# Performance work log

Measured on AMD Instinct MI355X. Metric: run time of the kernel, lower is better.

The kernel has to match this reference:

```python
import jax, jax.numpy as jnp
import numpy as np
import math

H = 512
NH = 8
HD = H // NH


def _lin_params(key, out_dim, in_dim):
    k1, k2 = jax.random.split(key)
    bound = 1.0 / math.sqrt(in_dim)
    w = jax.random.uniform(k1, (out_dim, in_dim), minval=-bound, maxval=bound, dtype=jnp.float32)
    b = jax.random.uniform(k2, (out_dim,), minval=-bound, maxval=bound, dtype=jnp.float32)
    return w, b


def setup_inputs() -> dict:
    key = jax.random.key(0)
    ks = jax.random.split(key, 16)
    B, L = 8, 1024
    inp = {
        'hidden_states': jax.random.normal(ks[0], (B, L, H), dtype=jnp.float32),
        'text': jax.random.normal(ks[1], (B, L, H), dtype=jnp.float32),
    }
    names = ['q_img', 'k_img', 'v_img', 'q_txt', 'k_txt', 'v_txt', 'out_img', 'out_txt']
    for i, n in enumerate(names):
        w, b = _lin_params(ks[2 + i], H, H)
        inp['w_' + n] = w
        inp['b_' + n] = b
    wcat, bcat = _lin_params(ks[10], H, 2 * H)
    inp['w_cat'] = wcat
    inp['b_cat'] = bcat
    # nn.MultiheadAttention params: in_proj [3H, H], out_proj [H, H]
    inp['in_proj_w'] = jax.random.normal(ks[11], (3 * H, H), dtype=jnp.float32) * (1.0 / math.sqrt(H))
    inp['in_proj_b'] = jnp.zeros((3 * H,), dtype=jnp.float32)
    pw, pb = _lin_params(ks[12], H, H)
    inp['out_proj_w'] = pw
    inp['out_proj_b'] = pb
    return inp


def _lin(x, w, b):
    return x @ w.T + b


def _heads(x):
    B, L, _ = x.shape
    return x.reshape(B, L, NH, HD).transpose(0, 2, 1, 3)  # [B, NH, L, HD]


def _attn(q, k, v):
    # q,k,v: [B, NH, L, HD]; dropout is identity in eval mode
    scores = jnp.einsum('bhqd,bhkd->bhqk', q, k) / math.sqrt(HD)
    probs = jax.nn.softmax(scores, axis=-1)
    ctx = jnp.einsum('bhqk,bhkd->bhqd', probs, v)
    B, _, L, _ = ctx.shape
    return ctx.transpose(0, 2, 1, 3).reshape(B, L, H)


def reference(hidden_states, text,
              w_q_img, b_q_img, w_k_img, b_k_img, w_v_img, b_v_img,
              w_q_txt, b_q_txt, w_k_txt, b_k_txt, w_v_txt, b_v_txt,
              w_out_img, b_out_img, w_out_txt, b_out_txt,
              w_cat, b_cat, in_proj_w, in_proj_b, out_proj_w, out_proj_b):
    q_img = _heads(_lin(hidden_states, w_q_img, b_q_img))
    k_img = _heads(_lin(hidden_states, w_k_img, b_k_img))
    v_img = _heads(_lin(hidden_states, w_v_img, b_v_img))
    q_txt = _heads(_lin(text, w_q_txt, b_q_txt))
    k_txt = _heads(_lin(text, w_k_txt, b_k_txt))
    v_txt = _heads(_lin(text, w_v_txt, b_v_txt))

    ctx_img = _attn(q_img, k_img, v_img)
    ctx_txt = _attn(q_txt, k_txt, v_txt)
    ctx_it = _attn(q_img, k_txt, v_txt)
    ctx_ti = _attn(q_txt, k_img, v_img)

    out_img = _lin((ctx_img + ctx_it) * 0.5, w_out_img, b_out_img)
    out_txt = _lin((ctx_txt + ctx_ti) * 0.5, w_out_txt, b_out_txt)
    out = _lin(jnp.concatenate([out_img, out_txt], axis=2), w_cat, b_cat)

    # attention pooling (nn.MultiheadAttention self-attention, batch-major math)
    qkv = _lin(out, in_proj_w, in_proj_b)
    q, k, v = jnp.split(qkv, 3, axis=-1)
    ctx = _attn(_heads(q), _heads(k), _heads(v))
    return _lin(ctx, out_proj_w, out_proj_b)
```

## Files before the change

### kernel.cpp

```cpp
#include <hip/hip_runtime.h>

typedef unsigned short u16;
typedef __attribute__((ext_vector_type(4))) unsigned short u16x4;
typedef __attribute__((ext_vector_type(8))) unsigned short u16x8;
typedef __attribute__((ext_vector_type(4))) float f32x4;
typedef __attribute__((ext_vector_type(8))) __bf16 bf16x8;
typedef __attribute__((ext_vector_type(2))) unsigned int u32x2;
typedef __attribute__((ext_vector_type(4))) unsigned int u32x4;

#define WS_XH    0UL
#define WS_XT    8388608UL
#define WS_W     16777216UL
#define WS_BQI   24117248UL
#define WS_BQT   24123392UL
#define WS_QKVI  24129536UL
#define WS_QKVT  49295360UL
#define WS_VTI   74461184UL
#define WS_VTT   82849792UL
#define WS_CTXIA 91238400UL
#define WS_CTXTA 99627008UL
#define WS_OCAT  108015616UL
#define WS_OUT2  24129536UL
#define WS_QKVP  32518144UL
#define WS_VTP   57683968UL
#define WS_CTXP  66072576UL

#define SCALE_LOG2E_O8 0.18033688011112042f

__device__ __forceinline__ u16 f2bf(float f) {
  unsigned u = __float_as_uint(f);
  u += 0x7fffu + ((u >> 16) & 1u);
  return (u16)(u >> 16);
}
__device__ __forceinline__ float bf2f(u16 v) {
  return __uint_as_float(((unsigned)v) << 16);
}
__device__ __forceinline__ bf16x8 as_bf(u16x8 v) { return __builtin_bit_cast(bf16x8, v); }
__device__ __forceinline__ f32x4 mfma16(bf16x8 a, bf16x8 b, f32x4 c) {
  return __builtin_amdgcn_mfma_f32_16x16x32_bf16(a, b, c, 0, 0, 0);
}
__device__ __forceinline__ unsigned cvt_pk_bf16(float lo, float hi) {
  unsigned r;
  asm("v_cvt_pk_bf16_f32 %0, %1, %2" : "=v"(r) : "v"(lo), "v"(hi));
  return r;
}
__device__ __forceinline__ void gl_lds16(const u16* g, u16* l) {
  __builtin_amdgcn_global_load_lds(
      (const __attribute__((address_space(1))) void*)g,
      (__attribute__((address_space(3))) void*)l, 16, 0, 0);
}

__global__ __launch_bounds__(256) void cvt_f32_bf16(const float* __restrict__ s0,
                                                    const float* __restrict__ s1,
                                                    u16* __restrict__ d0,
                                                    u16* __restrict__ d1, int n) {
  const float* s = blockIdx.y ? s1 : s0;
  u16* d = blockIdx.y ? d1 : d0;
  int i = (blockIdx.x * 256 + threadIdx.x) * 4;
  if (i >= n) return;
  float4 v = *(const float4*)(s + i);
  u16x4 o;
  o[0] = f2bf(v.x); o[1] = f2bf(v.y); o[2] = f2bf(v.z); o[3] = f2bf(v.w);
  *(u16x4*)(d + i) = o;
}

__global__ __launch_bounds__(256) void prep_weights(
    const float* __restrict__ wqi, const float* __restrict__ wki, const float* __restrict__ wvi,
    const float* __restrict__ wqt, const float* __restrict__ wkt, const float* __restrict__ wvt,
    const float* __restrict__ woi, const float* __restrict__ wot,
    const float* __restrict__ wc,  const float* __restrict__ wip, const float* __restrict__ wop,
    const float* __restrict__ bqi, const float* __restrict__ bki, const float* __restrict__ bvi,
    const float* __restrict__ bqt, const float* __restrict__ bkt, const float* __restrict__ bvt,
    u16* __restrict__ wdst, float* __restrict__ bi, float* __restrict__ bt) {
  int i = blockIdx.x * 256 + threadIdx.x;
  if (i < 786432) {
    const float* s = i < 262144 ? wqi : (i < 524288 ? wki : wvi);
    wdst[i] = f2bf(s[i & 262143]);
  } else if (i < 1572864) {
    int j = i - 786432;
    const float* s = j < 262144 ? wqt : (j < 524288 ? wkt : wvt);
    wdst[i] = f2bf(s[j & 262143]);
  } else if (i < 1835008) wdst[i] = f2bf(woi[i - 1572864]);
  else if (i < 2097152)   wdst[i] = f2bf(wot[i - 1835008]);
  else if (i < 2621440)   wdst[i] = f2bf(wc [i - 2097152]);
  else if (i < 3407872)   wdst[i] = f2bf(wip[i - 2621440]);
  else if (i < 3670016)   wdst[i] = f2bf(wop[i - 3407872]);
  else if (i < 3671552) {
    int j = i - 3670016;
    bi[j] = j < 512 ? bqi[j] : (j < 1024 ? bki[j - 512] : bvi[j - 1024]);
  } else if (i < 3673088) {
    int j = i - 3671552;
    bt[j] = j < 512 ? bqt[j] : (j < 1024 ? bkt[j - 512] : bvt[j - 1024]);
  }
}

__global__ __launch_bounds__(256) void gemm_bf16(
    const u16* __restrict__ A, const u16* __restrict__ A2, int lda,
    const u16* __restrict__ W,
    const float* __restrict__ bias, u16* __restrict__ C, int ldc, int coff, int K,
    int f32out, int qcols, float qscale, u16* __restrict__ vtout,
    long zdA, long zdA2, long zdW, long zdB, long zdC, long zdVT, int zdCoff) {
  if (blockIdx.z) {
    A += zdA;
    if (A2) A2 += zdA2;
    W += zdW; bias += zdB; C += zdC;
    if (vtout) vtout += zdVT;
    coff += zdCoff;
  }
  __shared__ __align__(16) u16 As[2][8 * 512];
  __shared__ __align__(16) u16 Bs[2][8 * 512];
  const int tid = threadIdx.x, lane = tid & 63, wv = tid >> 6;
  const int wm = wv >> 1, wn = wv & 1;
  const int ln15 = lane & 15;
  const int m0 = blockIdx.x * 128, n0 = blockIdx.y * 128;

  const int srow = lane & 15, skc = lane >> 4;
  const u16* gA0 = A + (long)(m0 + wv * 32 + srow) * lda + skc * 8;
  const u16* gA1 = gA0 + (long)16 * lda;
  const u16* gW0 = W + (long)(n0 + wv * 32 + srow) * K + skc * 8;
  const u16* gW1 = gW0 + (long)16 * K;

  f32x4 acc[4][4];
#pragma unroll
  for (int j = 0; j < 4; ++j) {
    float bv = bias[n0 + wn * 64 + j * 16 + ln15];
#pragma unroll
    for (int i = 0; i < 4; ++i) acc[i][j] = f32x4{bv, bv, bv, bv};
  }

  if (!A2) {
    {
      u16* la = As[0] + wv * 1024;
      u16* lb = Bs[0] + wv * 1024;
      gl_lds16(gA0, la);
      gl_lds16(gA1, la + 512);
      gl_lds16(gW0, lb);
      gl_lds16(gW1, lb + 512);
    }
    int cur = 0;
    for (int k0 = 0; k0 < K; k0 += 32, cur ^= 1) {
      __syncthreads();
      if (k0 + 32 < K) {
        u16* la = As[cur ^ 1] + wv * 1024;
        u16* lb = Bs[cur ^ 1] + wv * 1024;
        gl_lds16(gA0 + k0 + 32, la);
        gl_lds16(gA1 + k0 + 32, la + 512);
        gl_lds16(gW0 + k0 + 32, lb);
        gl_lds16(gW1 + k0 + 32, lb + 512);
      }
      bf16x8 af[4], bfr[4];
#pragma unroll
      for (int i = 0; i < 4; ++i)
        af[i] = as_bf(*(const u16x8*)(As[cur] + (wm * 4 + i) * 512 + lane * 8));
#pragma unroll
      for (int j = 0; j < 4; ++j)
        bfr[j] = as_bf(*(const u16x8*)(Bs[cur] + (wn * 4 + j) * 512 + lane * 8));
#pragma unroll
      for (int i = 0; i < 4; ++i)
#pragma unroll
        for (int j = 0; j < 4; ++j) acc[i][j] = mfma16(af[i], bfr[j], acc[i][j]);
    }
  } else {
    const u16* gA20 = A2 + (long)(m0 + wv * 32 + srow) * lda + skc * 8;
    const u16* gA21 = gA20 + (long)16 * lda;
    u16x8 ra0 = *(const u16x8*)(gA0);
    u16x8 ra1 = *(const u16x8*)(gA1);
    u16x8 rb0 = *(const u16x8*)(gW0);
    u16x8 rb1 = *(const u16x8*)(gW1);
    u16x8 rc0 = *(const u16x8*)(gA20);
    u16x8 rc1 = *(const u16x8*)(gA21);
    int buf = 0;
    for (int k0 = 0; k0 < K; k0 += 32, buf ^= 1) {
      u16x8 wa0 = ra0, wa1 = ra1;
#pragma unroll
      for (int u = 0; u < 8; ++u) {
        wa0[u] = f2bf(bf2f(ra0[u]) + bf2f(rc0[u]));
        wa1[u] = f2bf(bf2f(ra1[u]) + bf2f(rc1[u]));
      }
      u16* la = As[buf] + (wv * 2) * 512;
      u16* lb = Bs[buf] + (wv * 2) * 512;
      *(u16x8*)(la + lane * 8) = wa0;
      *(u16x8*)(la + 512 + lane * 8) = wa1;
      *(u16x8*)(lb + lane * 8) = rb0;
      *(u16x8*)(lb + 512 + lane * 8) = rb1;
      __syncthreads();
      if (k0 + 32 < K) {
        ra0 = *(const u16x8*)(gA0 + k0 + 32);
        ra1 = *(const u16x8*)(gA1 + k0 + 32);
        rb0 = *(const u16x8*)(gW0 + k0 + 32);
        rb1 = *(const u16x8*)(gW1 + k0 + 32);
        rc0 = *(const u16x8*)(gA20 + k0 + 32);
        rc1 = *(const u16x8*)(gA21 + k0 + 32);
      }
      bf16x8 af[4], bfr[4];
#pragma unroll
      for (int i = 0; i < 4; ++i)
        af[i] = as_bf(*(const u16x8*)(As[buf] + (wm * 4 + i) * 512 + lane * 8));
#pragma unroll
      for (int j = 0; j < 4; ++j)
        bfr[j] = as_bf(*(const u16x8*)(Bs[buf] + (wn * 4 + j) * 512 + lane * 8));
#pragma unroll
      for (int i = 0; i < 4; ++i)
#pragma unroll
        for (int j = 0; j < 4; ++j) acc[i][j] = mfma16(af[i], bfr[j], acc[i][j]);
    }
  }
  const int quad = lane >> 4;
  const int qr4 = quad * 4;
  if (vtout && n0 >= 1024) {
#pragma unroll
    for (int j = 0; j < 4; ++j) {
      int col = n0 + wn * 64 + j * 16 + ln15;
      int dg = col - 1024;
#pragma unroll
      for (int i = 0; i < 4; ++i) {
        int row0 = m0 + wm * 64 + i * 16 + qr4;
        long vr = ((long)(row0 >> 10) * 8 + (dg >> 6)) * 64 + (dg & 63);
        u16x4 ov;
#pragma unroll
        for (int r = 0; r < 4; ++r) ov[r] = f2bf(acc[i][j][r]);
        *(u16x4*)(vtout + vr * 1024 + (row0 & 1023)) = ov;
      }
    }
    return;
  }
  float colsc[4];
#pragma unroll
  for (int j = 0; j < 4; ++j)
    colsc[j] = (n0 + wn * 64 + j * 16 < qcols) ? qscale : 1.0f;
#pragma unroll
  for (int i = 0; i < 4; ++i)
#pragma unroll
    for (int r = 0; r < 4; ++r) {
      int row = m0 + wm * 64 + i * 16 + qr4 + r;
      long cidx = (long)row * ldc + coff + n0 + wn * 64 + ln15;
      if (f32out) {
        float* cf = (float*)C + cidx;
#pragma unroll
        for (int j = 0; j < 4; ++j) cf[j * 16] = acc[i][j][r] * colsc[j];
      } else {
        u16* cp = C + cidx;
#pragma unroll
        for (int j = 0; j < 4; ++j) cp[j * 16] = f2bf(acc[i][j][r] * colsc[j]);
      }
    }
}

template <int NQF, bool DUAL>
__global__ __launch_bounds__(256) void attn_flash(
    const u16* __restrict__ Q0, const u16* __restrict__ Q1, int ldq,
    const u16* __restrict__ K0, const u16* __restrict__ VT0,
    const u16* __restrict__ K1, const u16* __restrict__ VT1, int ldk,
    u16* __restrict__ O00, u16* __restrict__ O01,
    u16* __restrict__ O10, u16* __restrict__ O11, int ldo, float outscale) {
  __shared__ __align__(16) u16 Kt[2][32][72];
  __shared__ __align__(16) u16 Vt[2][64][40];
  const int tid = threadIdx.x, lane = tid & 63, wv = tid >> 6;
  const int ln15 = lane & 15, quad = lane >> 4, q8 = quad * 8;
  const int h = blockIdx.y;

  const u16 *Q, *K, *VT;
  u16* O;
  int qtile, b;
  if constexpr (DUAL) {
    qtile = blockIdx.x >> 1;
    const int phase = blockIdx.x & 1;
    const int qsel = blockIdx.z & 1;
    b = blockIdx.z >> 1;
    Q = qsel ? Q1 : Q0;
    const int ksel = qsel ^ phase;
    K = ksel ? K1 : K0;
    VT = ksel ? VT1 : VT0;
    O = qsel ? (phase ? O11 : O10) : (phase ? O01 : O00);
  } else {
    qtile = blockIdx.x;
    b = blockIdx.z;
    Q = Q0; K = K0; VT = VT0; O = O00;
  }
  const long qrow = (long)b * 1024 + qtile * (NQF * 64) + wv * (NQF * 16);

  bf16x8 qf[NQF][2];
#pragma unroll
  for (int qi = 0; qi < NQF; ++qi) {
    const u16* qp = Q + (qrow + qi * 16 + ln15) * ldq + h * 64;
    qf[qi][0] = as_bf(*(const u16x8*)(qp + q8));
    qf[qi][1] = as_bf(*(const u16x8*)(qp + 32 + q8));
  }

  u16x8 ones_u;
#pragma unroll
  for (int j = 0; j < 8; ++j) ones_u[j] = 0x3F80;
  const bf16x8 onesb = as_bf(ones_u);

  const int kk = tid >> 3, dc = (tid & 7) * 8;
  const int vd = tid >> 2;
  const int ko = (tid & 3) * 8;
  const int vs0 = ((tid & 1) << 4) | ((tid & 2) << 1);
  const u16* Kbase = K + ((long)b * 1024 + kk) * ldk + h * 64 + dc;
  const u16* Vbase = VT + ((long)((b * 8 + h) * 64 + vd)) * 1024 + ko;

  f32x4 o[NQF][4];
  f32x4 lacc[NQF];
#pragma unroll
  for (int qi = 0; qi < NQF; ++qi) {
    lacc[qi] = f32x4{0.f, 0.f, 0.f, 0.f};
#pragma unroll
    for (int j = 0; j < 4; ++j) o[qi][j] = f32x4{0.f, 0.f, 0.f, 0.f};
  }

  u32x4 kreg = *(const u32x4*)(Kbase);
  u32x4 vreg = *(const u32x4*)(Vbase);

  int cur = 0;
  for (int k0 = 0; k0 < 1024; k0 += 32, cur ^= 1) {
    *(u32x4*)(&Kt[cur][kk][dc]) = kreg;
    u32x2 vlo = {vreg[0], vreg[1]}, vhi = {vreg[2], vreg[3]};
    *(u32x2*)(&Vt[cur][vd][vs0]) = vlo;
    *(u32x2*)(&Vt[cur][vd][vs0 + 8]) = vhi;
    __syncthreads();
    if (k0 + 32 < 1024) {
      kreg = *(const u32x4*)(Kbase + (long)(k0 + 32) * ldk);
      vreg = *(const u32x4*)(Vbase + (k0 + 32));
    }

    f32x4 st[2][NQF];
#pragma unroll
    for (int kt = 0; kt < 2; ++kt) {
      bf16x8 ka0 = as_bf(*(const u16x8*)(&Kt[cur][kt * 16 + ln15][q8]));
      bf16x8 ka1 = as_bf(*(const u16x8*)(&Kt[cur][kt * 16 + ln15][32 + q8]));
#pragma unroll
      for (int qi = 0; qi < NQF; ++qi) {
        f32x4 z = f32x4{0.f, 0.f, 0.f, 0.f};
        z = mfma16(ka0, qf[qi][0], z);
        z = mfma16(ka1, qf[qi][1], z);
        st[kt][qi] = z;
      }
    }

    bf16x8 pb[NQF];
#pragma unroll
    for (int qi = 0; qi < NQF; ++qi) {
      float p00 = __builtin_amdgcn_exp2f(st[0][qi][0]);
      float p01 = __builtin_amdgcn_exp2f(st[0][qi][1]);
      float p02 = __builtin_amdgcn_exp2f(st[0][qi][2]);
      float p03 = __builtin_amdgcn_exp2f(st[0][qi][3]);
      float p10 = __builtin_amdgcn_exp2f(st[1][qi][0]);
      float p11 = __builtin_amdgcn_exp2f(st[1][qi][1]);
      float p12 = __builtin_amdgcn_exp2f(st[1][qi][2]);
      float p13 = __builtin_amdgcn_exp2f(st[1][qi][3]);
      u32x4 pk;
      pk[0] = cvt_pk_bf16(p00, p01);
      pk[1] = cvt_pk_bf16(p02, p03);
      pk[2] = cvt_pk_bf16(p10, p11);
      pk[3] = cvt_pk_bf16(p12, p13);
      pb[qi] = as_bf(__builtin_bit_cast(u16x8, pk));
      lacc[qi] = mfma16(onesb, pb[qi], lacc[qi]);
    }
#pragma unroll
    for (int j = 0; j < 4; ++j) {
      bf16x8 av = as_bf(*(const u16x8*)(&Vt[cur][j * 16 + ln15][q8]));
#pragma unroll
      for (int qi = 0; qi < NQF; ++qi) o[qi][j] = mfma16(av, pb[qi], o[qi][j]);
    }
  }

#pragma unroll
  for (int qi = 0; qi < NQF; ++qi) {
    float inv = outscale / lacc[qi][0];
    long row = qrow + qi * 16 + ln15;
#pragma unroll
    for (int j = 0; j < 4; ++j) {
      u16x4 ov;
#pragma unroll
      for (int r = 0; r < 4; ++r) ov[r] = f2bf(o[qi][j][r] * inv);
      *(u16x4*)(O + row * ldo + h * 64 + j * 16 + quad * 4) = ov;
    }
  }
}

extern "C" void kernel_launch(void* const* d_in, const int* in_sizes, int n_in,
                              void* d_out, int out_size, void* d_ws, size_t ws_size,
                              hipStream_t stream) {
  const float* hidden = (const float*)d_in[0];
  const float* text   = (const float*)d_in[1];
  const float* wqi = (const float*)d_in[2];  const float* bqi = (const float*)d_in[3];
  const float* wki = (const float*)d_in[4];  const float* bki = (const float*)d_in[5];
  const float* wvi = (const float*)d_in[6];  const float* bvi = (const float*)d_in[7];
  const float* wqt = (const float*)d_in[8];  const float* bqt = (const float*)d_in[9];
  const float* wkt = (const float*)d_in[10]; const float* bkt = (const float*)d_in[11];
  const float* wvt = (const float*)d_in[12]; const float* bvt = (const float*)d_in[13];
  const float* woi = (const float*)d_in[14]; const float* boi = (const float*)d_in[15];
  const float* wot = (const float*)d_in[16]; const float* bot = (const float*)d_in[17];
  const float* wc  = (const float*)d_in[18]; const float* bc  = (const float*)d_in[19];
  const float* wip = (const float*)d_in[20]; const float* bip = (const float*)d_in[21];
  const float* wop = (const float*)d_in[22]; const float* bop = (const float*)d_in[23];

  char* ws = (char*)d_ws;
  u16* XH    = (u16*)(ws + WS_XH);
  u16* XT    = (u16*)(ws + WS_XT);
  u16* WB    = (u16*)(ws + WS_W);
  float* BQI = (float*)(ws + WS_BQI);
  float* BQT = (float*)(ws + WS_BQT);
  u16* QKVI  = (u16*)(ws + WS_QKVI);
  u16* QKVT  = (u16*)(ws + WS_QKVT);
  u16* VTI   = (u16*)(ws + WS_VTI);
  u16* VTT   = (u16*)(ws + WS_VTT);
  u16* CTXIA = (u16*)(ws + WS_CTXIA);
  u16* CTXIB = (u16*)(ws + WS_XH);
  u16* CTXTA = (u16*)(ws + WS_CTXTA);
  u16* CTXTB = (u16*)(ws + WS_XT);
  u16* OCAT  = (u16*)(ws + WS_OCAT);
  u16* OUT2  = (u16*)(ws + WS_OUT2);
  u16* QKVP  = (u16*)(ws + WS_QKVP);
  u16* VTP   = (u16*)(ws + WS_VTP);
  u16* CTXP  = (u16*)(ws + WS_CTXP);

  u16* WQKVI = WB;
  u16* WOUTI = WB + 1572864;
  u16* WCAT  = WB + 2097152;
  u16* WINP  = WB + 2621440;
  u16* WOUTP = WB + 3407872;

  const int NACT = 8192 * 512;

  cvt_f32_bf16<<<dim3(NACT / 1024, 2), 256, 0, stream>>>(hidden, text, XH, XT, NACT);
  prep_weights<<<dim3(14348), 256, 0, stream>>>(wqi, wki, wvi, wqt, wkt, wvt, woi, wot,
                                                wc, wip, wop, bqi, bki, bvi, bqt, bkt, bvt,
                                                WB, BQI, BQT);
  gemm_bf16<<<dim3(64, 12, 2), 256, 0, stream>>>(
      XH, nullptr, 512, WQKVI, BQI, QKVI, 1536, 0, 512, 0, 512, SCALE_LOG2E_O8, VTI,
      4194304, 0, 786432, 1536, 12582912, 4194304, 0);
  attn_flash<4, true><<<dim3(8, 8, 16), 256, 0, stream>>>(
      QKVI, QKVT, 1536, QKVI + 512, VTI, QKVT + 512, VTT, 1536,
      CTXIA, CTXIB, CTXTA, CTXTB, 512, 0.5f);
  gemm_bf16<<<dim3(64, 4, 2), 256, 0, stream>>>(
      CTXIA, CTXIB, 512, WOUTI, boi, OCAT, 1024, 0, 512, 0, 0, 1.0f, nullptr,
      4194304, 4194304, 262144, (long)(bot - boi),
      0, 0, 512);
  gemm_bf16<<<dim3(64, 4, 1), 256, 0, stream>>>(
      OCAT, nullptr, 1024, WCAT, bc, OUT2, 512, 0, 1024, 0, 0, 1.0f, nullptr,
      0, 0, 0, 0, 0, 0, 0);
  gemm_bf16<<<dim3(64, 12, 1), 256, 0, stream>>>(
      OUT2, nullptr, 512, WINP, bip, QKVP, 1536, 0, 512, 0, 512, SCALE_LOG2E_O8, VTP,
      0, 0, 0, 0, 0, 0, 0);
  attn_flash<2, false><<<dim3(8, 8, 8), 256, 0, stream>>>(
      QKVP, nullptr, 1536, QKVP + 512, VTP, nullptr, nullptr, 1536,
      CTXP, nullptr, nullptr, nullptr, 512, 1.0f);
  gemm_bf16<<<dim3(64, 4, 1), 256, 0, stream>>>(
      CTXP, nullptr, 512, WOUTP, bop, (u16*)d_out, 512, 0, 512, 1, 0, 1.0f, nullptr,
      0, 0, 0, 0, 0, 0, 0);
}
```

Before: 397.9 us.

## Triple-buffer GEMM loads, add MFMA priority hints, halve attention query tile

The single-input GEMM path now uses a three-stage LDS ring with direct global-to-LDS loads. It waits on vmcnt(4) plus a raw barrier so two tiles stay in flight, replacing double buffering with a full __syncthreads. The flash attention loop wraps its MFMA sections in s_setprio to favour matrix issue across waves. The first attention launch drops from 4 to 2 query fragments per wave and doubles the grid in x to raise occupancy and parallelism. Risks include more LDS per block in the GEMM and reloading K/V twice as often per query in attention.

```diff
diff --git a/kernel.cpp b/kernel.cpp
--- a/kernel.cpp
+++ b/kernel.cpp
@@ -26,6 +26,7 @@
 #define WS_CTXP  66072576UL
 
 #define SCALE_LOG2E_O8 0.18033688011112042f
+
 
 __device__ __forceinline__ u16 f2bf(float f) {
   unsigned u = __float_as_uint(f);
@@ -94,6 +95,7 @@
   }
 }
 
+template <bool TRIPLE>
 __global__ __launch_bounds__(256) void gemm_bf16(
     const u16* __restrict__ A, const u16* __restrict__ A2, int lda,
     const u16* __restrict__ W,
@@ -107,8 +109,8 @@
     if (vtout) vtout += zdVT;
     coff += zdCoff;
   }
-  __shared__ __align__(16) u16 As[2][8 * 512];
-  __shared__ __align__(16) u16 Bs[2][8 * 512];
+  __shared__ __align__(16) u16 As[TRIPLE ? 3 : 2][8 * 512];
+  __shared__ __align__(16) u16 Bs[TRIPLE ? 3 : 2][8 * 512];
   const int tid = threadIdx.x, lane = tid & 63, wv = tid >> 6;
   const int wm = wv >> 1, wn = wv & 1;
   const int ln15 = lane & 15;
@@ -128,33 +130,46 @@
     for (int i = 0; i < 4; ++i) acc[i][j] = f32x4{bv, bv, bv, bv};
   }
 
-  if (!A2) {
+  if constexpr (TRIPLE) {
+    const int so = wv * 1024;
+    u16 *cA0 = As[0], *cA1 = As[1], *cA2 = As[2];
+    u16 *cB0 = Bs[0], *cB1 = Bs[1], *cB2 = Bs[2];
+    gl_lds16(gA0,      cA0 + so); gl_lds16(gA1,      cA0 + so + 512);
+    gl_lds16(gW0,      cB0 + so); gl_lds16(gW1,      cB0 + so + 512);
+    gl_lds16(gA0 + 32, cA1 + so); gl_lds16(gA1 + 32, cA1 + so + 512);
+    gl_lds16(gW0 + 32, cB1 + so); gl_lds16(gW1 + 32, cB1 + so + 512);
+    for (int k0 = 0; k0 < K - 32; k0 += 32) {
+      asm volatile("s_waitcnt vmcnt(4)\n\ts_barrier" ::: "memory");
+      __builtin_amdgcn_sched_barrier(0);
+      if (k0 + 64 < K) {
+        gl_lds16(gA0 + k0 + 64, cA2 + so); gl_lds16(gA1 + k0 + 64, cA2 + so + 512);
+        gl_lds16(gW0 + k0 + 64, cB2 + so); gl_lds16(gW1 + k0 + 64, cB2 + so + 512);
+      }
+      bf16x8 af[4], bfr[4];
+#pragma unroll
+      for (int i = 0; i < 4; ++i)
+        af[i] = as_bf(*(const u16x8*)(cA0 + (wm * 4 + i) * 512 + lane * 8));
+#pragma unroll
+      for (int j = 0; j < 4; ++j)
+        bfr[j] = as_bf(*(const u16x8*)(cB0 + (wn * 4 + j) * 512 + lane * 8));
+#pragma unroll
+      for (int i = 0; i < 4; ++i)
+#pragma unroll
+        for (int j = 0; j < 4; ++j) acc[i][j] = mfma16(af[i], bfr[j], acc[i][j]);
+      u16* t;
+      t = cA0; cA0 = cA1; cA1 = cA2; cA2 = t;
+      t = cB0; cB0 = cB1; cB1 = cB2; cB2 = t;
+    }
+    asm volatile("s_waitcnt vmcnt(0)\n\ts_barrier" ::: "memory");
+    __builtin_amdgcn_sched_barrier(0);
     {
-      u16* la = As[0] + wv * 1024;
-      u16* lb = Bs[0] + wv * 1024;
-      gl_lds16(gA0, la);
-      gl_lds16(gA1, la + 512);
-      gl_lds16(gW0, lb);
-      gl_lds16(gW1, lb + 512);
-    }
-    int cur = 0;
-    for (int k0 = 0; k0 < K; k0 += 32, cur ^= 1) {
-      __syncthreads();
-      if (k0 + 32 < K) {
-        u16* la = As[cur ^ 1] + wv * 1024;
-        u16* lb = Bs[cur ^ 1] + wv * 1024;
-        gl_lds16(gA0 + k0 + 32, la);
-        gl_lds16(gA1 + k0 + 32, la + 512);
-        gl_lds16(gW0 + k0 + 32, lb);
-        gl_lds16(gW1 + k0 + 32, lb + 512);
-      }
       bf16x8 af[4], bfr[4];
 #pragma unroll
       for (int i = 0; i < 4; ++i)
-        af[i] = as_bf(*(const u16x8*)(As[cur] + (wm * 4 + i) * 512 + lane * 8));
+        af[i] = as_bf(*(const u16x8*)(cA0 + (wm * 4 + i) * 512 + lane * 8));
 #pragma unroll
       for (int j = 0; j < 4; ++j)
-        bfr[j] = as_bf(*(const u16x8*)(Bs[cur] + (wn * 4 + j) * 512 + lane * 8));
+        bfr[j] = as_bf(*(const u16x8*)(cB0 + (wn * 4 + j) * 512 + lane * 8));
 #pragma unroll
       for (int i = 0; i < 4; ++i)
 #pragma unroll
@@ -171,7 +186,7 @@
     u16x8 rc1 = *(const u16x8*)(gA21);
     int buf = 0;
     for (int k0 = 0; k0 < K; k0 += 32, buf ^= 1) {
-      u16x8 wa0 = ra0, wa1 = ra1;
+      u16x8 wa0, wa1;
 #pragma unroll
       for (int u = 0; u < 8; ++u) {
         wa0[u] = f2bf(bf2f(ra0[u]) + bf2f(rc0[u]));
@@ -324,6 +339,7 @@
     }
 
     f32x4 st[2][NQF];
+    __builtin_amdgcn_s_setprio(1);
 #pragma unroll
     for (int kt = 0; kt < 2; ++kt) {
       bf16x8 ka0 = as_bf(*(const u16x8*)(&Kt[cur][kt * 16 + ln15][q8]));
@@ -336,6 +352,7 @@
         st[kt][qi] = z;
       }
     }
+    __builtin_amdgcn_s_setprio(0);
 
     bf16x8 pb[NQF];
 #pragma unroll
@@ -356,12 +373,14 @@
       pb[qi] = as_bf(__builtin_bit_cast(u16x8, pk));
       lacc[qi] = mfma16(onesb, pb[qi], lacc[qi]);
     }
+    __builtin_amdgcn_s_setprio(1);
 #pragma unroll
     for (int j = 0; j < 4; ++j) {
       bf16x8 av = as_bf(*(const u16x8*)(&Vt[cur][j * 16 + ln15][q8]));
 #pragma unroll
       for (int qi = 0; qi < NQF; ++qi) o[qi][j] = mfma16(av, pb[qi], o[qi][j]);
     }
+    __builtin_amdgcn_s_setprio(0);
   }
 
 #pragma unroll
@@ -427,26 +446,26 @@
   prep_weights<<<dim3(14348), 256, 0, stream>>>(wqi, wki, wvi, wqt, wkt, wvt, woi, wot,
                                                 wc, wip, wop, bqi, bki, bvi, bqt, bkt, bvt,
                                                 WB, BQI, BQT);
-  gemm_bf16<<<dim3(64, 12, 2), 256, 0, stream>>>(
+  gemm_bf16<true><<<dim3(64, 12, 2), 256, 0, stream>>>(
       XH, nullptr, 512, WQKVI, BQI, QKVI, 1536, 0, 512, 0, 512, SCALE_LOG2E_O8, VTI,
       4194304, 0, 786432, 1536, 12582912, 4194304, 0);
-  attn_flash<4, true><<<dim3(8, 8, 16), 256, 0, stream>>>(
+  attn_flash<2, true><<<dim3(16, 8, 16), 256, 0, stream>>>(
       QKVI, QKVT, 1536, QKVI + 512, VTI, QKVT + 512, VTT, 1536,
       CTXIA, CTXIB, CTXTA, CTXTB, 512, 0.5f);
-  gemm_bf16<<<dim3(64, 4, 2), 256, 0, stream>>>(
+  gemm_bf16<false><<<dim3(64, 4, 2), 256, 0, stream>>>(
       CTXIA, CTXIB, 512, WOUTI, boi, OCAT, 1024, 0, 512, 0, 0, 1.0f, nullptr,
       4194304, 4194304, 262144, (long)(bot - boi),
       0, 0, 512);
-  gemm_bf16<<<dim3(64, 4, 1), 256, 0, stream>>>(
+  gemm_bf16<true><<<dim3(64, 4, 1), 256, 0, stream>>>(
       OCAT, nullptr, 1024, WCAT, bc, OUT2, 512, 0, 1024, 0, 0, 1.0f, nullptr,
       0, 0, 0, 0, 0, 0, 0);
-  gemm_bf16<<<dim3(64, 12, 1), 256, 0, stream>>>(
+  gemm_bf16<true><<<dim3(64, 12, 1), 256, 0, stream>>>(
       OUT2, nullptr, 512, WINP, bip, QKVP, 1536, 0, 512, 0, 512, SCALE_LOG2E_O8, VTP,
       0, 0, 0, 0, 0, 0, 0);
   attn_flash<2, false><<<dim3(8, 8, 8), 256, 0, stream>>>(
       QKVP, nullptr, 1536, QKVP + 512, VTP, nullptr, nullptr, 1536,
       CTXP, nullptr, nullptr, nullptr, 512, 1.0f);
-  gemm_bf16<<<dim3(64, 4, 1), 256, 0, stream>>>(
+  gemm_bf16<true><<<dim3(64, 4, 1), 256, 0, stream>>>(
       CTXP, nullptr, 512, WOUTP, bop, (u16*)d_out, 512, 0, 512, 1, 0, 1.0f, nullptr,
       0, 0, 0, 0, 0, 0, 0);
 }
```

Result: faster. 381.7 us (-4.1%).
